# Kernel optimization log

Measured on AMD Instinct MI355X. Metric: run time of the kernel, lower is better.

The kernel has to match this reference:

```python
import jax, jax.numpy as jnp
import numpy as np

B, N = 8, 4096
DL = DR = DO = R = 256
SP = 3  # spatial tensor index dimension


def setup_inputs() -> dict:
    key = jax.random.key(0)
    k1, k2, k3, k4, k5 = jax.random.split(key, 5)
    x_l = jax.random.normal(k1, (B, N, DL, SP), dtype=jnp.float32)
    x_r = jax.random.normal(k2, (B, N, DR, SP), dtype=jnp.float32)
    # TensLinear self_init: normal with std = fan_in**-0.5
    W_l = jax.random.normal(k3, (R, DL), dtype=jnp.float32) * DL ** (-0.5)
    W_r = jax.random.normal(k4, (R, DR), dtype=jnp.float32) * DR ** (-0.5)
    W_o = jax.random.normal(k5, (DO, R), dtype=jnp.float32) * R ** (-0.5)
    return {"x_l": x_l, "x_r": x_r, "W_l": W_l, "W_r": W_r, "W_o": W_o}


def reference(x_l, x_r, W_l, W_r, W_o):
    # lin_l / lin_r: channel mixing into shared rank dim (tensor indices untouched)
    xl = jnp.einsum('OI,bnIi->bnOi', W_l, x_l)          # [B,N,R,3]
    xr = jnp.einsum('OI,bnIj->bnOj', W_r, x_r)          # [B,N,R,3]
    # inds_l=1, inds_r=1, inds_o=2 => contracts=0: outer product '...i,...j->...ij'
    xo = jnp.einsum('bnri,bnrj->bnrij', xl, xr)          # [B,N,R,3,3]
    # lin_o: mix rank -> dim_o
    return jnp.einsum('OI,bnIij->bnOij', W_o, xo)        # [B,N,DO,3,3]
```

## Files before the change

kernel.cpp:

```cpp
#include <hip/hip_runtime.h>

typedef short bf16x8 __attribute__((ext_vector_type(8)));
typedef float f32x4 __attribute__((ext_vector_type(4)));

__device__ inline unsigned short f2bf(float f) {
    union { float f; unsigned u; } v; v.f = f;
    unsigned u = v.u;
    u += 0x7fffu + ((u >> 16) & 1u);
    return (unsigned short)(u >> 16);
}

#define KPAD 264

__global__ void prep_weights(const float* __restrict__ wl,
                             const float* __restrict__ wr,
                             const float* __restrict__ wo,
                             unsigned short* __restrict__ wsw) {
    int idx = blockIdx.x * 256 + threadIdx.x;
    int w    = idx >> 16;
    int e    = idx & 65535;
    int jj   = e & 7;
    int lane = (e >> 3) & 63;
    int kmt  = e >> 9;
    int ks   = kmt & 7;
    int mt   = kmt >> 3;
    int row = mt * 16 + (lane & 15);
    int col = ks * 32 + (lane >> 4) * 8 + jj;
    const float* src = (w == 0) ? wl : (w == 1) ? wr : wo;
    wsw[idx] = f2bf(src[row * 256 + col]);
}

__global__ __launch_bounds__(512, 4) void fused_kernel(
    const float* __restrict__ xl_g, const float* __restrict__ xr_g,
    const unsigned short* __restrict__ wsw, float* __restrict__ out) {

    __shared__ __align__(16) unsigned short lds[38016];

    const int tid  = threadIdx.x;
    const int blk  = blockIdx.x;
    const int wave = tid >> 6;
    const int lane = tid & 63;
    const int q    = lane >> 4;
    const int l15  = lane & 15;

    const float* srcs[2] = { xl_g + (size_t)blk * 12288, xr_g + (size_t)blk * 12288 };
    for (int a = 0; a < 2; ++a) {
        const float4* s4 = (const float4*)srcs[a];
        unsigned short* dst = lds + a * 12672;
        #pragma unroll
        for (int it = 0; it < 6; ++it) {
            int g4 = it * 512 + tid;
            float4 v = s4[g4];
            int g = g4 * 4;
            int tok = g / 768;
            int m0 = g - tok * 768;
            float vv[4] = {v.x, v.y, v.z, v.w};
            #pragma unroll
            for (int e = 0; e < 4; ++e) {
                int mm = m0 + e;
                int I = mm / 3;
                int i = mm - I * 3;
                dst[(i * 16 + tok) * KPAD + I] = f2bf(vv[e]);
            }
        }
    }
    __syncthreads();

    const bf16x8* wlf = (const bf16x8*)(wsw);
    const bf16x8* wrf = (const bf16x8*)(wsw + 65536);
    const bf16x8* wof = (const bf16x8*)(wsw + 131072);

    f32x4 accL[2][3] = {};
    f32x4 accR[2][3] = {};

    #pragma unroll
    for (int k = 0; k < 8; ++k) {
        const int koff = k * 32 + q * 8;
        bf16x8 bl[3], br[3];
        #pragma unroll
        for (int nt = 0; nt < 3; ++nt) {
            bl[nt] = *(const bf16x8*)&lds[(nt * 16 + l15) * KPAD + koff];
            br[nt] = *(const bf16x8*)&lds[12672 + (nt * 16 + l15) * KPAD + koff];
        }
        #pragma unroll
        for (int m = 0; m < 2; ++m) {
            const int mt = wave * 2 + m;
            bf16x8 al = wlf[(mt * 8 + k) * 64 + lane];
            bf16x8 ar = wrf[(mt * 8 + k) * 64 + lane];
            #pragma unroll
            for (int nt = 0; nt < 3; ++nt) {
                accL[m][nt] = __builtin_amdgcn_mfma_f32_16x16x32_bf16(al, bl[nt], accL[m][nt], 0, 0, 0);
                accR[m][nt] = __builtin_amdgcn_mfma_f32_16x16x32_bf16(ar, br[nt], accR[m][nt], 0, 0, 0);
            }
        }
    }
    __syncthreads();

    #pragma unroll
    for (int m = 0; m < 2; ++m) {
        const int mt = wave * 2 + m;
        const int r0 = mt * 16 + q * 4;
        #pragma unroll
        for (int i = 0; i < 3; ++i) {
            #pragma unroll
            for (int j = 0; j < 3; ++j) {
                const int c = (i * 3 + j) * 16 + l15;
                unsigned short h[4];
                #pragma unroll
                for (int reg = 0; reg < 4; ++reg)
                    h[reg] = f2bf(accL[m][i][reg] * accR[m][j][reg]);
                uint2 pk;
                pk.x = (unsigned)h[0] | ((unsigned)h[1] << 16);
                pk.y = (unsigned)h[2] | ((unsigned)h[3] << 16);
                *(uint2*)&lds[c * KPAD + r0] = pk;
            }
        }
    }
    __syncthreads();

    f32x4 accA[2][5] = {};
    f32x4 accB[2][4] = {};
    #pragma unroll
    for (int k = 0; k < 8; ++k) {
        const int koff = k * 32 + q * 8;
        bf16x8 pf[5];
        #pragma unroll
        for (int p = 0; p < 5; ++p)
            pf[p] = *(const bf16x8*)&lds[(p * 16 + l15) * KPAD + koff];
        #pragma unroll
        for (int m = 0; m < 2; ++m) {
            const int mt = wave * 2 + m;
            bf16x8 ao = wof[(mt * 8 + k) * 64 + lane];
            #pragma unroll
            for (int p = 0; p < 5; ++p)
                accA[m][p] = __builtin_amdgcn_mfma_f32_16x16x32_bf16(ao, pf[p], accA[m][p], 0, 0, 0);
        }
    }
    #pragma unroll
    for (int k = 0; k < 8; ++k) {
        const int koff = k * 32 + q * 8;
        bf16x8 pf[4];
        #pragma unroll
        for (int p = 0; p < 4; ++p)
            pf[p] = *(const bf16x8*)&lds[((5 + p) * 16 + l15) * KPAD + koff];
        #pragma unroll
        for (int m = 0; m < 2; ++m) {
            const int mt = wave * 2 + m;
            bf16x8 ao = wof[(mt * 8 + k) * 64 + lane];
            #pragma unroll
            for (int p = 0; p < 4; ++p)
                accB[m][p] = __builtin_amdgcn_mfma_f32_16x16x32_bf16(ao, pf[p], accB[m][p], 0, 0, 0);
        }
    }
    __syncthreads();

    float* sf = (float*)(lds + wave * 4736);
    const int tok = lane >> 2, sub = lane & 3;
    #pragma unroll
    for (int m = 0; m < 2; ++m) {
        const int mt = wave * 2 + m;
        #pragma unroll
        for (int reg = 0; reg < 4; ++reg) {
            const int o9 = (q * 4 + reg) * 9;
            #pragma unroll
            for (int p = 0; p < 9; ++p) {
                float v = (p < 5) ? accA[m][p][reg] : accB[m][p - 5][reg];
                sf[l15 * 148 + o9 + p] = v;
            }
        }
        __syncthreads();
        float* wdst = out + ((size_t)blk * 16 + tok) * 2304 + mt * 144;
        #pragma unroll
        for (int it = 0; it < 9; ++it) {
            const int f4 = sub + 4 * it;
            float4 v = *(const float4*)&sf[tok * 148 + f4 * 4];
            ((float4*)wdst)[f4] = v;
        }
        __syncthreads();
    }
}

extern "C" void kernel_launch(void* const* d_in, const int* in_sizes, int n_in,
                              void* d_out, int out_size, void* d_ws, size_t ws_size,
                              hipStream_t stream) {
    const float* xl = (const float*)d_in[0];
    const float* xr = (const float*)d_in[1];
    const float* wl = (const float*)d_in[2];
    const float* wr = (const float*)d_in[3];
    const float* wo = (const float*)d_in[4];
    float* out = (float*)d_out;
    unsigned short* wsw = (unsigned short*)d_ws;

    prep_weights<<<768, 256, 0, stream>>>(wl, wr, wo, wsw);
    fused_kernel<<<2048, 512, 0, stream>>>(xl, xr, wsw, out);
}
```

Measured before the change: 486.3 us.

## Make fused kernel persistent with register-prefetch of next token group inputs

Launches 512 persistent blocks that each process four 16-token groups in a loop instead of one block per group. The next group's x_l and x_r float4 values are loaded into registers during the current group's MFMA and store phases, so global load latency can overlap compute. This adds 48 live registers per thread for the prefetch buffers, which may reduce occupancy under the 512x4 launch bounds. It also halves the grid relative to the CU count times blocks per CU, which may leave some compute idle.

```diff
diff --git a/kernel.cpp b/kernel.cpp
--- a/kernel.cpp
+++ b/kernel.cpp
@@ -11,6 +11,8 @@
 }
 
 #define KPAD 264
+#define GPB  4
+#define NBLK 512
 
 __global__ void prep_weights(const float* __restrict__ wl,
                              const float* __restrict__ wr,
@@ -37,146 +39,171 @@
     __shared__ __align__(16) unsigned short lds[38016];
 
     const int tid  = threadIdx.x;
-    const int blk  = blockIdx.x;
     const int wave = tid >> 6;
     const int lane = tid & 63;
     const int q    = lane >> 4;
     const int l15  = lane & 15;
 
-    const float* srcs[2] = { xl_g + (size_t)blk * 12288, xr_g + (size_t)blk * 12288 };
-    for (int a = 0; a < 2; ++a) {
-        const float4* s4 = (const float4*)srcs[a];
-        unsigned short* dst = lds + a * 12672;
-        #pragma unroll
-        for (int it = 0; it < 6; ++it) {
-            int g4 = it * 512 + tid;
-            float4 v = s4[g4];
-            int g = g4 * 4;
-            int tok = g / 768;
-            int m0 = g - tok * 768;
-            float vv[4] = {v.x, v.y, v.z, v.w};
-            #pragma unroll
-            for (int e = 0; e < 4; ++e) {
-                int mm = m0 + e;
-                int I = mm / 3;
-                int i = mm - I * 3;
-                dst[(i * 16 + tok) * KPAD + I] = f2bf(vv[e]);
-            }
-        }
-    }
-    __syncthreads();
-
+    const float4* L4 = (const float4*)xl_g;
+    const float4* R4 = (const float4*)xr_g;
     const bf16x8* wlf = (const bf16x8*)(wsw);
     const bf16x8* wrf = (const bf16x8*)(wsw + 65536);
     const bf16x8* wof = (const bf16x8*)(wsw + 131072);
 
-    f32x4 accL[2][3] = {};
-    f32x4 accR[2][3] = {};
-
-    #pragma unroll
-    for (int k = 0; k < 8; ++k) {
-        const int koff = k * 32 + q * 8;
-        bf16x8 bl[3], br[3];
-        #pragma unroll
-        for (int nt = 0; nt < 3; ++nt) {
-            bl[nt] = *(const bf16x8*)&lds[(nt * 16 + l15) * KPAD + koff];
-            br[nt] = *(const bf16x8*)&lds[12672 + (nt * 16 + l15) * KPAD + koff];
-        }
+    int g = blockIdx.x;
+    float4 preL[6], preR[6];
+    {
+        const size_t base = (size_t)g * 3072;
+        #pragma unroll
+        for (int u = 0; u < 6; ++u) preL[u] = L4[base + u * 512 + tid];
+        #pragma unroll
+        for (int u = 0; u < 6; ++u) preR[u] = R4[base + u * 512 + tid];
+    }
+
+    for (int itg = 0; itg < GPB; ++itg) {
+        const int gn = g + NBLK;
+        const size_t nbase = (size_t)gn * 3072;
+
+        #pragma unroll
+        for (int a = 0; a < 2; ++a) {
+            unsigned short* dst = lds + a * 12672;
+            #pragma unroll
+            for (int u = 0; u < 6; ++u) {
+                float4 v = a ? preR[u] : preL[u];
+                int g4 = u * 512 + tid;
+                int gi = g4 * 4;
+                int tok = gi / 768;
+                int m0 = gi - tok * 768;
+                float vv[4] = {v.x, v.y, v.z, v.w};
+                #pragma unroll
+                for (int e = 0; e < 4; ++e) {
+                    int mm = m0 + e;
+                    int I = mm / 3;
+                    int i = mm - I * 3;
+                    dst[(i * 16 + tok) * KPAD + I] = f2bf(vv[e]);
+                }
+            }
+        }
+        __syncthreads();
+
+        if (itg != GPB - 1) {
+            #pragma unroll
+            for (int u = 0; u < 6; ++u) preL[u] = L4[nbase + u * 512 + tid];
+        }
+
+        f32x4 accL[2][3] = {};
+        f32x4 accR[2][3] = {};
+        #pragma unroll
+        for (int k = 0; k < 8; ++k) {
+            const int koff = k * 32 + q * 8;
+            bf16x8 bl[3], br[3];
+            #pragma unroll
+            for (int nt = 0; nt < 3; ++nt) {
+                bl[nt] = *(const bf16x8*)&lds[(nt * 16 + l15) * KPAD + koff];
+                br[nt] = *(const bf16x8*)&lds[12672 + (nt * 16 + l15) * KPAD + koff];
+            }
+            #pragma unroll
+            for (int m = 0; m < 2; ++m) {
+                const int mt = wave * 2 + m;
+                bf16x8 al = wlf[(mt * 8 + k) * 64 + lane];
+                bf16x8 ar = wrf[(mt * 8 + k) * 64 + lane];
+                #pragma unroll
+                for (int nt = 0; nt < 3; ++nt) {
+                    accL[m][nt] = __builtin_amdgcn_mfma_f32_16x16x32_bf16(al, bl[nt], accL[m][nt], 0, 0, 0);
+                    accR[m][nt] = __builtin_amdgcn_mfma_f32_16x16x32_bf16(ar, br[nt], accR[m][nt], 0, 0, 0);
+                }
+            }
+        }
+        __syncthreads();
+
         #pragma unroll
         for (int m = 0; m < 2; ++m) {
             const int mt = wave * 2 + m;
-            bf16x8 al = wlf[(mt * 8 + k) * 64 + lane];
-            bf16x8 ar = wrf[(mt * 8 + k) * 64 + lane];
-            #pragma unroll
-            for (int nt = 0; nt < 3; ++nt) {
-                accL[m][nt] = __builtin_amdgcn_mfma_f32_16x16x32_bf16(al, bl[nt], accL[m][nt], 0, 0, 0);
-                accR[m][nt] = __builtin_amdgcn_mfma_f32_16x16x32_bf16(ar, br[nt], accR[m][nt], 0, 0, 0);
-            }
-        }
-    }
-    __syncthreads();
-
-    #pragma unroll
-    for (int m = 0; m < 2; ++m) {
-        const int mt = wave * 2 + m;
-        const int r0 = mt * 16 + q * 4;
-        #pragma unroll
-        for (int i = 0; i < 3; ++i) {
-            #pragma unroll
-            for (int j = 0; j < 3; ++j) {
-                const int c = (i * 3 + j) * 16 + l15;
-                unsigned short h[4];
-                #pragma unroll
-                for (int reg = 0; reg < 4; ++reg)
-                    h[reg] = f2bf(accL[m][i][reg] * accR[m][j][reg]);
-                uint2 pk;
-                pk.x = (unsigned)h[0] | ((unsigned)h[1] << 16);
-                pk.y = (unsigned)h[2] | ((unsigned)h[3] << 16);
-                *(uint2*)&lds[c * KPAD + r0] = pk;
-            }
-        }
-    }
-    __syncthreads();
-
-    f32x4 accA[2][5] = {};
-    f32x4 accB[2][4] = {};
-    #pragma unroll
-    for (int k = 0; k < 8; ++k) {
-        const int koff = k * 32 + q * 8;
-        bf16x8 pf[5];
-        #pragma unroll
-        for (int p = 0; p < 5; ++p)
-            pf[p] = *(const bf16x8*)&lds[(p * 16 + l15) * KPAD + koff];
+            const int r0 = mt * 16 + q * 4;
+            #pragma unroll
+            for (int i = 0; i < 3; ++i) {
+                #pragma unroll
+                for (int j = 0; j < 3; ++j) {
+                    const int c = (i * 3 + j) * 16 + l15;
+                    unsigned short h[4];
+                    #pragma unroll
+                    for (int reg = 0; reg < 4; ++reg)
+                        h[reg] = f2bf(accL[m][i][reg] * accR[m][j][reg]);
+                    uint2 pk;
+                    pk.x = (unsigned)h[0] | ((unsigned)h[1] << 16);
+                    pk.y = (unsigned)h[2] | ((unsigned)h[3] << 16);
+                    *(uint2*)&lds[c * KPAD + r0] = pk;
+                }
+            }
+        }
+        __syncthreads();
+
+        f32x4 accA[2][5] = {};
+        f32x4 accB[2][4] = {};
+        #pragma unroll
+        for (int k = 0; k < 8; ++k) {
+            const int koff = k * 32 + q * 8;
+            bf16x8 pf[5];
+            #pragma unroll
+            for (int p = 0; p < 5; ++p)
+                pf[p] = *(const bf16x8*)&lds[(p * 16 + l15) * KPAD + koff];
+            #pragma unroll
+            for (int m = 0; m < 2; ++m) {
+                const int mt = wave * 2 + m;
+                bf16x8 ao = wof[(mt * 8 + k) * 64 + lane];
+                #pragma unroll
+                for (int p = 0; p < 5; ++p)
+                    accA[m][p] = __builtin_amdgcn_mfma_f32_16x16x32_bf16(ao, pf[p], accA[m][p], 0, 0, 0);
+            }
+        }
+        #pragma unroll
+        for (int k = 0; k < 8; ++k) {
+            const int koff = k * 32 + q * 8;
+            bf16x8 pf[4];
+            #pragma unroll
+            for (int p = 0; p < 4; ++p)
+                pf[p] = *(const bf16x8*)&lds[((5 + p) * 16 + l15) * KPAD + koff];
+            #pragma unroll
+            for (int m = 0; m < 2; ++m) {
+                const int mt = wave * 2 + m;
+                bf16x8 ao = wof[(mt * 8 + k) * 64 + lane];
+                #pragma unroll
+                for (int p = 0; p < 4; ++p)
+                    accB[m][p] = __builtin_amdgcn_mfma_f32_16x16x32_bf16(ao, pf[p], accB[m][p], 0, 0, 0);
+            }
+        }
+        __syncthreads();
+
+        float* sf = (float*)(lds + wave * 4736);
+        const int tok2 = lane >> 2, sub = lane & 3;
         #pragma unroll
         for (int m = 0; m < 2; ++m) {
             const int mt = wave * 2 + m;
-            bf16x8 ao = wof[(mt * 8 + k) * 64 + lane];
-            #pragma unroll
-            for (int p = 0; p < 5; ++p)
-                accA[m][p] = __builtin_amdgcn_mfma_f32_16x16x32_bf16(ao, pf[p], accA[m][p], 0, 0, 0);
-        }
-    }
-    #pragma unroll
-    for (int k = 0; k < 8; ++k) {
-        const int koff = k * 32 + q * 8;
-        bf16x8 pf[4];
-        #pragma unroll
-        for (int p = 0; p < 4; ++p)
-            pf[p] = *(const bf16x8*)&lds[((5 + p) * 16 + l15) * KPAD + koff];
-        #pragma unroll
-        for (int m = 0; m < 2; ++m) {
-            const int mt = wave * 2 + m;
-            bf16x8 ao = wof[(mt * 8 + k) * 64 + lane];
-            #pragma unroll
-            for (int p = 0; p < 4; ++p)
-                accB[m][p] = __builtin_amdgcn_mfma_f32_16x16x32_bf16(ao, pf[p], accB[m][p], 0, 0, 0);
-        }
-    }
-    __syncthreads();
-
-    float* sf = (float*)(lds + wave * 4736);
-    const int tok = lane >> 2, sub = lane & 3;
-    #pragma unroll
-    for (int m = 0; m < 2; ++m) {
-        const int mt = wave * 2 + m;
-        #pragma unroll
-        for (int reg = 0; reg < 4; ++reg) {
-            const int o9 = (q * 4 + reg) * 9;
-            #pragma unroll
-            for (int p = 0; p < 9; ++p) {
-                float v = (p < 5) ? accA[m][p][reg] : accB[m][p - 5][reg];
-                sf[l15 * 148 + o9 + p] = v;
-            }
-        }
-        __syncthreads();
-        float* wdst = out + ((size_t)blk * 16 + tok) * 2304 + mt * 144;
-        #pragma unroll
-        for (int it = 0; it < 9; ++it) {
-            const int f4 = sub + 4 * it;
-            float4 v = *(const float4*)&sf[tok * 148 + f4 * 4];
-            ((float4*)wdst)[f4] = v;
-        }
-        __syncthreads();
+            #pragma unroll
+            for (int reg = 0; reg < 4; ++reg) {
+                const int o9 = (q * 4 + reg) * 9;
+                #pragma unroll
+                for (int p = 0; p < 9; ++p) {
+                    float v = (p < 5) ? accA[m][p][reg] : accB[m][p - 5][reg];
+                    sf[l15 * 148 + o9 + p] = v;
+                }
+            }
+            __syncthreads();
+            float* wdst = out + ((size_t)g * 16 + tok2) * 2304 + mt * 144;
+            #pragma unroll
+            for (int it = 0; it < 9; ++it) {
+                const int f4 = sub + 4 * it;
+                float4 v = *(const float4*)&sf[tok2 * 148 + f4 * 4];
+                ((float4*)wdst)[f4] = v;
+            }
+            __syncthreads();
+
+            if (m == 0 && itg != GPB - 1) {
+                #pragma unroll
+                for (int u = 0; u < 6; ++u) preR[u] = R4[nbase + u * 512 + tid];
+            }
+        }
+        g = gn;
     }
 }
 
@@ -192,5 +219,5 @@
     unsigned short* wsw = (unsigned short*)d_ws;
 
     prep_weights<<<768, 256, 0, stream>>>(wl, wr, wo, wsw);
-    fused_kernel<<<2048, 512, 0, stream>>>(xl, xr, wsw, out);
-}
+    fused_kernel<<<NBLK, 512, 0, stream>>>(xl, xr, wsw, out);
+}
```

New measurement: 780.2 us. 1.6x slower.

## Swizzle LDS layout, batch global loads, vectorize staging and drop epilogue barriers

Applied to the files above, without the earlier changes.

Replaces the padded LDS row stride with an XOR-swizzled 256-wide layout, which also shrinks the shared buffer slightly. The input staging now has each thread issue all twelve float4 global loads up front. It converts each 4-channel group and writes it to LDS as one packed 8-byte store, replacing per-element scalar stores with divides. The epilogue writes accumulators to LDS as float4 and removes the block-wide barriers, relying on each wave owning its own staging region. The aim is to cut LDS bank conflicts, instruction overhead and synchronization stalls, at the cost of more registers held during the load phase.

```diff
diff --git a/kernel.cpp b/kernel.cpp
--- a/kernel.cpp
+++ b/kernel.cpp
@@ -10,7 +10,7 @@
     return (unsigned short)(u >> 16);
 }
 
-#define KPAD 264
+#define SWZ(row, s) (((row) << 8) | ((s) ^ (((row) & 7) << 3)))
 
 __global__ void prep_weights(const float* __restrict__ wl,
                              const float* __restrict__ wr,
@@ -34,7 +34,7 @@
     const float* __restrict__ xl_g, const float* __restrict__ xr_g,
     const unsigned short* __restrict__ wsw, float* __restrict__ out) {
 
-    __shared__ __align__(16) unsigned short lds[38016];
+    __shared__ __align__(16) unsigned short lds[37888];
 
     const int tid  = threadIdx.x;
     const int blk  = blockIdx.x;
@@ -43,24 +43,43 @@
     const int q    = lane >> 4;
     const int l15  = lane & 15;
 
-    const float* srcs[2] = { xl_g + (size_t)blk * 12288, xr_g + (size_t)blk * 12288 };
-    for (int a = 0; a < 2; ++a) {
-        const float4* s4 = (const float4*)srcs[a];
-        unsigned short* dst = lds + a * 12672;
-        #pragma unroll
-        for (int it = 0; it < 6; ++it) {
-            int g4 = it * 512 + tid;
-            float4 v = s4[g4];
-            int g = g4 * 4;
-            int tok = g / 768;
-            int m0 = g - tok * 768;
-            float vv[4] = {v.x, v.y, v.z, v.w};
-            #pragma unroll
-            for (int e = 0; e < 4; ++e) {
-                int mm = m0 + e;
-                int I = mm / 3;
-                int i = mm - I * 3;
-                dst[(i * 16 + tok) * KPAD + I] = f2bf(vv[e]);
+    {
+        const float4* p0 = (const float4*)(xl_g + (size_t)blk * 12288);
+        const float4* p1 = (const float4*)(xr_g + (size_t)blk * 12288);
+        const int tok0 = tid >> 6;
+        const int tok1 = 8 + tok0;
+        const int c0   = tid & 63;
+        const int I0   = c0 * 4;
+        float4 ld[12];
+        #pragma unroll
+        for (int u = 0; u < 3; ++u) ld[u]     = p0[tok0 * 192 + c0 * 3 + u];
+        #pragma unroll
+        for (int u = 0; u < 3; ++u) ld[3 + u] = p0[tok1 * 192 + c0 * 3 + u];
+        #pragma unroll
+        for (int u = 0; u < 3; ++u) ld[6 + u] = p1[tok0 * 192 + c0 * 3 + u];
+        #pragma unroll
+        for (int u = 0; u < 3; ++u) ld[9 + u] = p1[tok1 * 192 + c0 * 3 + u];
+        #pragma unroll
+        for (int a = 0; a < 2; ++a) {
+            unsigned short* dst = lds + a * 12288;
+            #pragma unroll
+            for (int s = 0; s < 2; ++s) {
+                const int tok = s ? tok1 : tok0;
+                float f[12];
+                #pragma unroll
+                for (int u = 0; u < 3; ++u) {
+                    float4 v = ld[a * 6 + s * 3 + u];
+                    f[u * 4 + 0] = v.x; f[u * 4 + 1] = v.y;
+                    f[u * 4 + 2] = v.z; f[u * 4 + 3] = v.w;
+                }
+                #pragma unroll
+                for (int c = 0; c < 3; ++c) {
+                    const int row = c * 16 + tok;
+                    uint2 pk;
+                    pk.x = (unsigned)f2bf(f[c])     | ((unsigned)f2bf(f[3 + c]) << 16);
+                    pk.y = (unsigned)f2bf(f[6 + c]) | ((unsigned)f2bf(f[9 + c]) << 16);
+                    *(uint2*)&dst[SWZ(row, I0)] = pk;
+                }
             }
         }
     }
@@ -72,15 +91,15 @@
 
     f32x4 accL[2][3] = {};
     f32x4 accR[2][3] = {};
-
     #pragma unroll
     for (int k = 0; k < 8; ++k) {
         const int koff = k * 32 + q * 8;
         bf16x8 bl[3], br[3];
         #pragma unroll
         for (int nt = 0; nt < 3; ++nt) {
-            bl[nt] = *(const bf16x8*)&lds[(nt * 16 + l15) * KPAD + koff];
-            br[nt] = *(const bf16x8*)&lds[12672 + (nt * 16 + l15) * KPAD + koff];
+            const int row = nt * 16 + l15;
+            bl[nt] = *(const bf16x8*)&lds[SWZ(row, koff)];
+            br[nt] = *(const bf16x8*)&lds[12288 + SWZ(row, koff)];
         }
         #pragma unroll
         for (int m = 0; m < 2; ++m) {
@@ -112,7 +131,7 @@
                 uint2 pk;
                 pk.x = (unsigned)h[0] | ((unsigned)h[1] << 16);
                 pk.y = (unsigned)h[2] | ((unsigned)h[3] << 16);
-                *(uint2*)&lds[c * KPAD + r0] = pk;
+                *(uint2*)&lds[SWZ(c, r0)] = pk;
             }
         }
     }
@@ -126,7 +145,7 @@
         bf16x8 pf[5];
         #pragma unroll
         for (int p = 0; p < 5; ++p)
-            pf[p] = *(const bf16x8*)&lds[(p * 16 + l15) * KPAD + koff];
+            pf[p] = *(const bf16x8*)&lds[SWZ(p * 16 + l15, koff)];
         #pragma unroll
         for (int m = 0; m < 2; ++m) {
             const int mt = wave * 2 + m;
@@ -142,7 +161,7 @@
         bf16x8 pf[4];
         #pragma unroll
         for (int p = 0; p < 4; ++p)
-            pf[p] = *(const bf16x8*)&lds[((5 + p) * 16 + l15) * KPAD + koff];
+            pf[p] = *(const bf16x8*)&lds[SWZ((5 + p) * 16 + l15, koff)];
         #pragma unroll
         for (int m = 0; m < 2; ++m) {
             const int mt = wave * 2 + m;
@@ -154,29 +173,32 @@
     }
     __syncthreads();
 
-    float* sf = (float*)(lds + wave * 4736);
-    const int tok = lane >> 2, sub = lane & 3;
+    float* sfw = (float*)lds + wave * 2368;
+    const int tok2 = lane >> 2, sub = lane & 3;
     #pragma unroll
     for (int m = 0; m < 2; ++m) {
         const int mt = wave * 2 + m;
-        #pragma unroll
-        for (int reg = 0; reg < 4; ++reg) {
-            const int o9 = (q * 4 + reg) * 9;
-            #pragma unroll
-            for (int p = 0; p < 9; ++p) {
-                float v = (p < 5) ? accA[m][p][reg] : accB[m][p - 5][reg];
-                sf[l15 * 148 + o9 + p] = v;
-            }
-        }
-        __syncthreads();
-        float* wdst = out + ((size_t)blk * 16 + tok) * 2304 + mt * 144;
+        float vf[36];
+        #pragma unroll
+        for (int reg = 0; reg < 4; ++reg)
+            #pragma unroll
+            for (int p = 0; p < 9; ++p)
+                vf[reg * 9 + p] = (p < 5) ? accA[m][p][reg] : accB[m][p - 5][reg];
+        float* wbase = sfw + l15 * 148 + q * 36;
+        #pragma unroll
+        for (int w = 0; w < 9; ++w) {
+            float4 t;
+            t.x = vf[4 * w]; t.y = vf[4 * w + 1];
+            t.z = vf[4 * w + 2]; t.w = vf[4 * w + 3];
+            *(float4*)&wbase[4 * w] = t;
+        }
+        float* wdst = out + ((size_t)blk * 16 + tok2) * 2304 + mt * 144;
         #pragma unroll
         for (int it = 0; it < 9; ++it) {
-            const int f4 = sub + 4 * it;
-            float4 v = *(const float4*)&sf[tok * 148 + f4 * 4];
-            ((float4*)wdst)[f4] = v;
-        }
-        __syncthreads();
+            const int f4i = sub + 4 * it;
+            float4 v = *(const float4*)&sfw[tok2 * 148 + f4i * 4];
+            ((float4*)wdst)[f4i] = v;
+        }
     }
 }
 
```

After: 501.8 us. 3.2% more time.
